# Performance work log

Measured on AMD Instinct MI355X. Metric: run time of the kernel, lower is better.

## Reference

```python
import jax, jax.numpy as jnp
import numpy as np

HID = 10  # hidden_dim


def conv1x1(x, w, b=None):
    # x: [N,C,H,W], w: [O,C] -> [N,O,H,W]
    y = jnp.einsum('oc,nchw->nohw', w, x)
    if b is not None:
        y = y + b[None, :, None, None]
    return y


def gconv1x1(x, w, b=None):
    # grouped 1x1 conv. x: [N,G*ipg,H,W], w: [G,opg,ipg]
    N, C, H, W = x.shape
    G, opg, ipg = w.shape
    xg = x.reshape(N, G, ipg, H, W)
    y = jnp.einsum('goi,ngihw->ngohw', w, xg).reshape(N, G * opg, H, W)
    if b is not None:
        y = y + b[None, :, None, None]
    return y


def _decomp(h_fea, xf, xh, att_w, att_b, w):
    # Decomposition: spatial attention from (fea, xf, xh), gate xf, project.
    att = jax.nn.sigmoid(conv1x1(jnp.concatenate([h_fea, xf, xh], axis=1), att_w, att_b))
    xfh = jax.nn.relu(conv1x1(xf * att, w))
    return xfh, att


def _comp(parts, xh, att_w, att_b, w):
    # Composition: parts [P,N,HID,H,W]; grouped per-part attention then fuse with xh.
    ca = jax.nn.sigmoid(jnp.einsum('pc,pnchw->pnhw', att_w[:, 0], parts) + att_b[:, None, None, None])
    msg = (parts * ca[:, :, None]).sum(0)  # [N,HID,H,W]
    return jax.nn.relu(conv1x1(jnp.concatenate([xh, msg], axis=1), w))


def _update(xh, m0, m1, m2, gate_w, gate_b, cand_w):
    # conv_Update: gated residual update from summed messages.
    cat = jnp.concatenate([xh, m0 + m1 + m2], axis=1)
    g = jax.nn.sigmoid(conv1x1(cat, gate_w, gate_b))
    cand = jax.nn.relu(conv1x1(cat, cand_w))
    return xh * (1.0 - g) + cand * g


def half_graph(h_fea, xh_u, xh_l, xf, xp, pdp_w1, pdp_w2, att_w, att_b,
               compU_att_w, compU_att_b, compU_w,
               compL_att_w, compL_att_b, compL_w,
               decU_att_w, decU_att_b, decU_w,
               decL_att_w, decL_att_b, decL_w,
               updU_gate_w, updU_gate_b, updU_cand_w,
               updL_gate_w, updL_gate_b, updL_cand_w):
    # Part_Dependency: shared trunk then grouped conv -> (dp_u, dp_l)
    t = jax.nn.relu(conv1x1(jnp.concatenate([h_fea, xh_u, xh_l], axis=1), pdp_w1))
    dp = jax.nn.relu(gconv1x1(t, pdp_w2))
    dp_u, dp_l = dp[:, :HID], dp[:, HID:]
    # grouped sigmoid attention over the two half nodes
    a = jax.nn.sigmoid(gconv1x1(jnp.concatenate([xh_u, xh_l], axis=1), att_w, att_b))
    ag_u, ag_l = a[:, 0:1], a[:, 1:2]
    # upper half node
    xphu = _comp(xp[0:4], xh_u, compU_att_w, compU_att_b, compU_w)
    xlh = dp_l * ag_l + xh_u * ag_u  # Pair_Part_Dependency (lower -> upper)
    xfhu, att_u = _decomp(h_fea, xf, xh_u, decU_att_w, decU_att_b, decU_w)
    xh_u_new = _update(xh_u, xphu, xlh, xfhu, updU_gate_w, updU_gate_b, updU_cand_w)
    # lower half node
    xphl = _comp(xp[4:6], xh_l, compL_att_w, compL_att_b, compL_w)
    xuh = dp_u * ag_u + xh_l * ag_l  # Pair_Part_Dependency (upper -> lower)
    xfhl, att_l = _decomp(h_fea, xf, xh_l, decL_att_w, decL_att_b, decL_w)
    xh_l_new = _update(xh_l, xphl, xuh, xfhl, updL_gate_w, updL_gate_b, updL_cand_w)
    return xh_u_new, xh_l_new, att_u, att_l


def setup_inputs() -> dict:
    key = jax.random.key(0)
    N, C, H, W = 8, 256, 128, 128
    ks = jax.random.split(key, 32)
    s = 0.05
    inp = {
        'h_fea': jax.random.normal(ks[0], (N, C, H, W), jnp.float32),
        'xh_u': jax.random.normal(ks[1], (N, HID, H, W), jnp.float32),
        'xh_l': jax.random.normal(ks[2], (N, HID, H, W), jnp.float32),
        'xf': jax.random.normal(ks[3], (N, HID, H, W), jnp.float32),
        'xp': jax.random.normal(ks[4], (6, N, HID, H, W), jnp.float32),
        'pdp_w1': jax.random.normal(ks[5], (2 * HID, C + 2 * HID), jnp.float32) * s,
        'pdp_w2': jax.random.normal(ks[6], (2, HID, HID), jnp.float32) * s,
        'att_w': jax.random.normal(ks[7], (2, 1, HID), jnp.float32) * s,
        'att_b': jnp.zeros((2,), jnp.float32),
        'compU_att_w': jax.random.normal(ks[8], (4, 1, HID), jnp.float32) * s,
        'compU_att_b': jnp.zeros((4,), jnp.float32),
        'compU_w': jax.random.normal(ks[9], (HID, 2 * HID), jnp.float32) * s,
        'compL_att_w': jax.random.normal(ks[10], (2, 1, HID), jnp.float32) * s,
        'compL_att_b': jnp.zeros((2,), jnp.float32),
        'compL_w': jax.random.normal(ks[11], (HID, 2 * HID), jnp.float32) * s,
        'decU_att_w': jax.random.normal(ks[12], (1, C + 2 * HID), jnp.float32) * s,
        'decU_att_b': jnp.zeros((1,), jnp.float32),
        'decU_w': jax.random.normal(ks[13], (HID, HID), jnp.float32) * s,
        'decL_att_w': jax.random.normal(ks[14], (1, C + 2 * HID), jnp.float32) * s,
        'decL_att_b': jnp.zeros((1,), jnp.float32),
        'decL_w': jax.random.normal(ks[15], (HID, HID), jnp.float32) * s,
        'updU_gate_w': jax.random.normal(ks[16], (HID, 2 * HID), jnp.float32) * s,
        'updU_gate_b': jnp.zeros((HID,), jnp.float32),
        'updU_cand_w': jax.random.normal(ks[17], (HID, 2 * HID), jnp.float32) * s,
        'updL_gate_w': jax.random.normal(ks[18], (HID, 2 * HID), jnp.float32) * s,
        'updL_gate_b': jnp.zeros((HID,), jnp.float32),
        'updL_cand_w': jax.random.normal(ks[19], (HID, 2 * HID), jnp.float32) * s,
    }
    return inp


def reference(h_fea, xh_u, xh_l, xf, xp, pdp_w1, pdp_w2, att_w, att_b,
              compU_att_w, compU_att_b, compU_w,
              compL_att_w, compL_att_b, compL_w,
              decU_att_w, decU_att_b, decU_w,
              decL_att_w, decL_att_b, decL_w,
              updU_gate_w, updU_gate_b, updU_cand_w,
              updL_gate_w, updL_gate_b, updL_cand_w):
    return half_graph(h_fea, xh_u, xh_l, xf, xp, pdp_w1, pdp_w2, att_w, att_b,
                      compU_att_w, compU_att_b, compU_w,
                      compL_att_w, compL_att_b, compL_w,
                      decU_att_w, decU_att_b, decU_w,
                      decL_att_w, decL_att_b, decL_w,
                      updU_gate_w, updU_gate_b, updU_cand_w,
                      updL_gate_w, updL_gate_b, updL_cand_w)
```

## Files before the change

### kernel.cpp

```cpp
#include <hip/hip_runtime.h>
#include <stdint.h>

typedef unsigned short u16;
typedef unsigned int   u32;

#define HW   16384
#define NPIX 131072

__device__ __forceinline__ float sigm(float x) { return 1.f / (1.f + __expf(-x)); }

__device__ __forceinline__ float rdlane(float v, int lane) {
    return __int_as_float(__builtin_amdgcn_readlane(__float_as_int(v), lane));
}

__global__ __launch_bounds__(256, 2) void half_graph_fused(
    const float* __restrict__ hf,  const float* __restrict__ xhu, const float* __restrict__ xhl,
    const float* __restrict__ xfg, const float* __restrict__ xpg,
    const float* __restrict__ pdp_w1, const float* __restrict__ pdp_w2,
    const float* __restrict__ att_w,  const float* __restrict__ att_b,
    const float* __restrict__ cU_aw, const float* __restrict__ cU_ab, const float* __restrict__ cU_w,
    const float* __restrict__ cL_aw, const float* __restrict__ cL_ab, const float* __restrict__ cL_w,
    const float* __restrict__ dU_aw, const float* __restrict__ dU_ab, const float* __restrict__ dU_w,
    const float* __restrict__ dL_aw, const float* __restrict__ dL_ab, const float* __restrict__ dL_w,
    const float* __restrict__ uU_gw, const float* __restrict__ uU_gb, const float* __restrict__ uU_cw,
    const float* __restrict__ uL_gw, const float* __restrict__ uL_gb, const float* __restrict__ uL_cw,
    float* __restrict__ out)
{
    const int p  = blockIdx.x * blockDim.x + threadIdx.x;
    const int n  = p >> 14;
    const int hw = p & 16383;
    const int ln = threadIdx.x & 63;

    float xu[10], xl[10], xv[10];
    {
        const float* a = xhu + (size_t)n * 10 * HW + hw;
        const float* b = xhl + (size_t)n * 10 * HW + hw;
        const float* c = xfg + (size_t)n * 10 * HW + hw;
        #pragma unroll
        for (int i = 0; i < 10; ++i) xu[i] = a[i * HW];
        #pragma unroll
        for (int i = 0; i < 10; ++i) xl[i] = b[i * HW];
        #pragma unroll
        for (int i = 0; i < 10; ++i) xv[i] = c[i * HW];
    }

    const float* hfp = hf + (size_t)n * 256 * HW + hw;

    float acc[22];
    #pragma unroll
    for (int o = 0; o < 22; ++o) acc[o] = 0.f;

    float wA[22], wB[22];
    auto prefetch = [&](float (&w)[22], int c0) {
        #pragma unroll
        for (int o = 0; o < 20; ++o) w[o] = pdp_w1[o * 276 + c0 + ln];
        w[20] = dU_aw[c0 + ln];
        w[21] = dL_aw[c0 + ln];
    };
    auto compute = [&](const float (&w)[22], int c0) {
        const float* xp0 = hfp + (size_t)c0 * HW;
        #pragma unroll 8
        for (int cc = 0; cc < 64; ++cc) {
            float x = xp0[cc * HW];
            #pragma unroll
            for (int o = 0; o < 22; ++o)
                acc[o] = fmaf(rdlane(w[o], cc), x, acc[o]);
        }
    };

    prefetch(wA, 0);
    prefetch(wB, 64);
    compute(wA, 0);
    prefetch(wA, 128);
    compute(wB, 64);
    prefetch(wB, 192);
    compute(wA, 128);
    compute(wB, 192);

    const float dU = acc[20], dL = acc[21];

    float t[20];
    #pragma unroll
    for (int o = 0; o < 20; ++o) {
        float s = acc[o];
        #pragma unroll
        for (int i = 0; i < 10; ++i) s = fmaf(pdp_w1[o * 276 + 256 + i], xu[i], s);
        #pragma unroll
        for (int i = 0; i < 10; ++i) s = fmaf(pdp_w1[o * 276 + 266 + i], xl[i], s);
        t[o] = fmaxf(s, 0.f);
    }
    float dpv[20];
    #pragma unroll
    for (int g = 0; g < 2; ++g) {
        #pragma unroll
        for (int o = 0; o < 10; ++o) {
            float s = 0.f;
            #pragma unroll
            for (int i = 0; i < 10; ++i)
                s = fmaf(pdp_w2[(g * 10 + o) * 10 + i], t[g * 10 + i], s);
            dpv[g * 10 + o] = fmaxf(s, 0.f);
        }
    }

    float au_s = att_b[0], al_s = att_b[1];
    #pragma unroll
    for (int i = 0; i < 10; ++i) {
        au_s = fmaf(att_w[i], xu[i], au_s);
        al_s = fmaf(att_w[10 + i], xl[i], al_s);
    }
    const float au = sigm(au_s), al = sigm(al_s);

    float su = dU + dU_ab[0];
    float sl = dL + dL_ab[0];
    #pragma unroll
    for (int i = 0; i < 10; ++i) { su = fmaf(dU_aw[256 + i], xv[i], su); sl = fmaf(dL_aw[256 + i], xv[i], sl); }
    #pragma unroll
    for (int i = 0; i < 10; ++i) { su = fmaf(dU_aw[266 + i], xu[i], su); sl = fmaf(dL_aw[266 + i], xl[i], sl); }
    const float attU = sigm(su), attL = sigm(sl);

    float xfhu[10], xfhl[10];
    #pragma unroll
    for (int o = 0; o < 10; ++o) {
        float a = 0.f, b = 0.f;
        #pragma unroll
        for (int i = 0; i < 10; ++i) {
            a = fmaf(dU_w[o * 10 + i], xv[i], a);
            b = fmaf(dL_w[o * 10 + i], xv[i], b);
        }
        xfhu[o] = fmaxf(attU * a, 0.f);
        xfhl[o] = fmaxf(attL * b, 0.f);
    }

    float msgU[10];
    #pragma unroll
    for (int i = 0; i < 10; ++i) msgU[i] = 0.f;
    #pragma unroll
    for (int pp = 0; pp < 4; ++pp) {
        const float* xq = xpg + (size_t)(pp * 8 + n) * 10 * HW + hw;
        float v[10];
        #pragma unroll
        for (int i = 0; i < 10; ++i) v[i] = xq[i * HW];
        float s = cU_ab[pp];
        #pragma unroll
        for (int i = 0; i < 10; ++i) s = fmaf(cU_aw[pp * 10 + i], v[i], s);
        float ca = sigm(s);
        #pragma unroll
        for (int i = 0; i < 10; ++i) msgU[i] = fmaf(ca, v[i], msgU[i]);
    }
    float xphu[10];
    #pragma unroll
    for (int o = 0; o < 10; ++o) {
        float s = 0.f;
        #pragma unroll
        for (int i = 0; i < 10; ++i) s = fmaf(cU_w[o * 20 + i], xu[i], s);
        #pragma unroll
        for (int i = 0; i < 10; ++i) s = fmaf(cU_w[o * 20 + 10 + i], msgU[i], s);
        xphu[o] = fmaxf(s, 0.f);
    }

    float msgL[10];
    #pragma unroll
    for (int i = 0; i < 10; ++i) msgL[i] = 0.f;
    #pragma unroll
    for (int pp = 4; pp < 6; ++pp) {
        const float* xq = xpg + (size_t)(pp * 8 + n) * 10 * HW + hw;
        float v[10];
        #pragma unroll
        for (int i = 0; i < 10; ++i) v[i] = xq[i * HW];
        float s = cL_ab[pp - 4];
        #pragma unroll
        for (int i = 0; i < 10; ++i) s = fmaf(cL_aw[(pp - 4) * 10 + i], v[i], s);
        float ca = sigm(s);
        #pragma unroll
        for (int i = 0; i < 10; ++i) msgL[i] = fmaf(ca, v[i], msgL[i]);
    }
    float xphl[10];
    #pragma unroll
    for (int o = 0; o < 10; ++o) {
        float s = 0.f;
        #pragma unroll
        for (int i = 0; i < 10; ++i) s = fmaf(cL_w[o * 20 + i], xl[i], s);
        #pragma unroll
        for (int i = 0; i < 10; ++i) s = fmaf(cL_w[o * 20 + 10 + i], msgL[i], s);
        xphl[o] = fmaxf(s, 0.f);
    }

    float outU[10], outL[10];
    {
        float m[10];
        #pragma unroll
        for (int i = 0; i < 10; ++i)
            m[i] = xphu[i] + (dpv[10 + i] * al + xu[i] * au) + xfhu[i];
        #pragma unroll
        for (int o = 0; o < 10; ++o) {
            float gs = uU_gb[o], cs = 0.f;
            #pragma unroll
            for (int i = 0; i < 10; ++i) {
                gs = fmaf(uU_gw[o * 20 + i], xu[i], gs);
                cs = fmaf(uU_cw[o * 20 + i], xu[i], cs);
            }
            #pragma unroll
            for (int i = 0; i < 10; ++i) {
                gs = fmaf(uU_gw[o * 20 + 10 + i], m[i], gs);
                cs = fmaf(uU_cw[o * 20 + 10 + i], m[i], cs);
            }
            float g = sigm(gs), cd = fmaxf(cs, 0.f);
            outU[o] = xu[o] * (1.f - g) + cd * g;
        }
    }
    {
        float m[10];
        #pragma unroll
        for (int i = 0; i < 10; ++i)
            m[i] = xphl[i] + (dpv[i] * au + xl[i] * al) + xfhl[i];
        #pragma unroll
        for (int o = 0; o < 10; ++o) {
            float gs = uL_gb[o], cs = 0.f;
            #pragma unroll
            for (int i = 0; i < 10; ++i) {
                gs = fmaf(uL_gw[o * 20 + i], xl[i], gs);
                cs = fmaf(uL_cw[o * 20 + i], xl[i], cs);
            }
            #pragma unroll
            for (int i = 0; i < 10; ++i) {
                gs = fmaf(uL_gw[o * 20 + 10 + i], m[i], gs);
                cs = fmaf(uL_cw[o * 20 + 10 + i], m[i], cs);
            }
            float g = sigm(gs), cd = fmaxf(cs, 0.f);
            outL[o] = xl[o] * (1.f - g) + cd * g;
        }
    }

    {
        int baseU = n * 10 * HW + hw;
        #pragma unroll
        for (int c = 0; c < 10; ++c) out[baseU + c * HW] = outU[c];
        int baseL = 1310720 + baseU;
        #pragma unroll
        for (int c = 0; c < 10; ++c) out[baseL + c * HW] = outL[c];
        out[2621440 + n * HW + hw] = attU;
        out[2752512 + n * HW + hw] = attL;
    }
}

extern "C" void kernel_launch(void* const* d_in, const int* in_sizes, int n_in,
                              void* d_out, int out_size, void* d_ws, size_t ws_size,
                              hipStream_t stream) {
    (void)in_sizes; (void)n_in; (void)out_size; (void)d_ws; (void)ws_size;
    const float* hf   = (const float*)d_in[0];
    const float* xhu  = (const float*)d_in[1];
    const float* xhl  = (const float*)d_in[2];
    const float* xfg  = (const float*)d_in[3];
    const float* xpg  = (const float*)d_in[4];
    const float* w1   = (const float*)d_in[5];
    const float* w2   = (const float*)d_in[6];
    const float* aw   = (const float*)d_in[7];
    const float* ab   = (const float*)d_in[8];
    const float* cUaw = (const float*)d_in[9];
    const float* cUab = (const float*)d_in[10];
    const float* cUw  = (const float*)d_in[11];
    const float* cLaw = (const float*)d_in[12];
    const float* cLab = (const float*)d_in[13];
    const float* cLw  = (const float*)d_in[14];
    const float* dUaw = (const float*)d_in[15];
    const float* dUab = (const float*)d_in[16];
    const float* dUw  = (const float*)d_in[17];
    const float* dLaw = (const float*)d_in[18];
    const float* dLab = (const float*)d_in[19];
    const float* dLw  = (const float*)d_in[20];
    const float* uUgw = (const float*)d_in[21];
    const float* uUgb = (const float*)d_in[22];
    const float* uUcw = (const float*)d_in[23];
    const float* uLgw = (const float*)d_in[24];
    const float* uLgb = (const float*)d_in[25];
    const float* uLcw = (const float*)d_in[26];

    dim3 grid(NPIX / 256), block(256);
    hipLaunchKernelGGL(half_graph_fused, grid, block, 0, stream,
        hf, xhu, xhl, xfg, xpg, w1, w2, aw, ab,
        cUaw, cUab, cUw, cLaw, cLab, cLw,
        dUaw, dUab, dUw, dLaw, dLab, dLw,
        uUgw, uUgb, uUcw, uLgw, uLgb, uLcw,
        (float*)d_out);
}
```

Before: 298.4 us.

## Use split-fp16 MFMA for 256-channel trunk and split upper/lower work across threads

The 256-channel 1x1 conv over h_fea (22 outputs) moves from scalar FMAs with readlane broadcasts onto 32x32x16 fp16 MFMA. Weights are pre-packed into hi/lo fp16 pairs by a small prep kernel, and activations are split on the fly, using three MFMAs per step to approximate fp32 accuracy. Results pass through shared memory to the epilogue, where each pixel's upper and lower branches are handled by two different threads, halving per-thread register pressure and allowing more waves per SIMD. Costs include an extra kernel launch, workspace use, a block barrier, and error from the split-fp16 approximation.

Result: faster. 278.3 us (-6.7%).

```diff
diff --git a/kernel.cpp b/kernel.cpp
--- a/kernel.cpp
+++ b/kernel.cpp
@@ -1,19 +1,35 @@
 #include <hip/hip_runtime.h>
 #include <stdint.h>
 
+typedef unsigned int   u32;
 typedef unsigned short u16;
-typedef unsigned int   u32;
-
-#define HW   16384
-#define NPIX 131072
+
+#define HW 16384
+
+typedef __attribute__((ext_vector_type(8)))  _Float16 half8;
+typedef __attribute__((ext_vector_type(16))) float    f32x16;
 
 __device__ __forceinline__ float sigm(float x) { return 1.f / (1.f + __expf(-x)); }
 
-__device__ __forceinline__ float rdlane(float v, int lane) {
-    return __int_as_float(__builtin_amdgcn_readlane(__float_as_int(v), lane));
+
+__global__ __launch_bounds__(256) void prep_apack(
+    const float* __restrict__ pdp_w1, const float* __restrict__ dU_aw,
+    const float* __restrict__ dL_aw, _Float16* __restrict__ apack)
+{
+    int idx = blockIdx.x * 256 + threadIdx.x;
+    int s = idx >> 9, rem = idx & 511, l = rem >> 3, j = rem & 7;
+    int o = l & 31, kh = l >> 5;
+    int k = s * 16 + kh * 8 + j;
+    float wv = 0.f;
+    if (o < 20)       wv = pdp_w1[o * 276 + k];
+    else if (o == 20) wv = dU_aw[k];
+    else if (o == 21) wv = dL_aw[k];
+    _Float16 h = (_Float16)wv;
+    apack[idx]        = h;
+    apack[8192 + idx] = (_Float16)(wv - (float)h);
 }
 
-__global__ __launch_bounds__(256, 2) void half_graph_fused(
+__global__ __launch_bounds__(256, 4) void half_graph_fused(
     const float* __restrict__ hf,  const float* __restrict__ xhu, const float* __restrict__ xhl,
     const float* __restrict__ xfg, const float* __restrict__ xpg,
     const float* __restrict__ pdp_w1, const float* __restrict__ pdp_w2,
@@ -24,173 +40,133 @@
     const float* __restrict__ dL_aw, const float* __restrict__ dL_ab, const float* __restrict__ dL_w,
     const float* __restrict__ uU_gw, const float* __restrict__ uU_gb, const float* __restrict__ uU_cw,
     const float* __restrict__ uL_gw, const float* __restrict__ uL_gb, const float* __restrict__ uL_cw,
+    const _Float16* __restrict__ apack,
     float* __restrict__ out)
 {
-    const int p  = blockIdx.x * blockDim.x + threadIdx.x;
-    const int n  = p >> 14;
-    const int hw = p & 16383;
-    const int ln = threadIdx.x & 63;
-
+    const int tid    = threadIdx.x;
+    const int pxbase = blockIdx.x * 128;
+    const int n      = pxbase >> 14;
+    const int hwbase = pxbase & 16383;
+
+    __shared__ float sacc[22][128];
+
+    {
+        const int l   = tid & 63;
+        const int w   = tid >> 6;
+        const int col = l & 31;
+        const int kh  = l >> 5;
+        const float* bp = hf + ((size_t)n * 256 + kh * 8) * HW + (hwbase + w * 32 + col);
+        const half8* ah  = (const half8*)apack;
+        const half8* al8 = ah + 1024;
+        f32x16 acc = {};
+        #pragma unroll 2
+        for (int s = 0; s < 16; ++s) {
+            half8 A_h = ah[s * 64 + l];
+            half8 A_l = al8[s * 64 + l];
+            float x[8];
+            #pragma unroll
+            for (int j = 0; j < 8; ++j) x[j] = bp[(size_t)(s * 16 + j) * HW];
+            half8 B_h, B_l;
+            #pragma unroll
+            for (int j = 0; j < 8; ++j) {
+                _Float16 h = (_Float16)x[j];
+                B_h[j] = h;
+                B_l[j] = (_Float16)(x[j] - (float)h);
+            }
+            acc = __builtin_amdgcn_mfma_f32_32x32x16_f16(A_h, B_h, acc, 0, 0, 0);
+            acc = __builtin_amdgcn_mfma_f32_32x32x16_f16(A_h, B_l, acc, 0, 0, 0);
+            acc = __builtin_amdgcn_mfma_f32_32x32x16_f16(A_l, B_h, acc, 0, 0, 0);
+        }
+        const int ccol = w * 32 + col;
+        #pragma unroll
+        for (int reg = 0; reg < 12; ++reg) {
+            const int r = (reg & 3) + 8 * (reg >> 2) + 4 * kh;
+            if (r < 22) sacc[r][ccol] = acc[reg];
+        }
+    }
+
+    const int q    = tid & 127;
+    const int role = tid >> 7;
+    const int hw   = hwbase + q;
+    const int vb   = n * 10 * HW + hw;
     float xu[10], xl[10], xv[10];
-    {
-        const float* a = xhu + (size_t)n * 10 * HW + hw;
-        const float* b = xhl + (size_t)n * 10 * HW + hw;
-        const float* c = xfg + (size_t)n * 10 * HW + hw;
-        #pragma unroll
-        for (int i = 0; i < 10; ++i) xu[i] = a[i * HW];
-        #pragma unroll
-        for (int i = 0; i < 10; ++i) xl[i] = b[i * HW];
-        #pragma unroll
-        for (int i = 0; i < 10; ++i) xv[i] = c[i * HW];
-    }
-
-    const float* hfp = hf + (size_t)n * 256 * HW + hw;
-
-    float acc[22];
     #pragma unroll
-    for (int o = 0; o < 22; ++o) acc[o] = 0.f;
-
-    float wA[22], wB[22];
-    auto prefetch = [&](float (&w)[22], int c0) {
-        #pragma unroll
-        for (int o = 0; o < 20; ++o) w[o] = pdp_w1[o * 276 + c0 + ln];
-        w[20] = dU_aw[c0 + ln];
-        w[21] = dL_aw[c0 + ln];
-    };
-    auto compute = [&](const float (&w)[22], int c0) {
-        const float* xp0 = hfp + (size_t)c0 * HW;
-        #pragma unroll 8
-        for (int cc = 0; cc < 64; ++cc) {
-            float x = xp0[cc * HW];
-            #pragma unroll
-            for (int o = 0; o < 22; ++o)
-                acc[o] = fmaf(rdlane(w[o], cc), x, acc[o]);
-        }
-    };
-
-    prefetch(wA, 0);
-    prefetch(wB, 64);
-    compute(wA, 0);
-    prefetch(wA, 128);
-    compute(wB, 64);
-    prefetch(wB, 192);
-    compute(wA, 128);
-    compute(wB, 192);
-
-    const float dU = acc[20], dL = acc[21];
-
-    float t[20];
+    for (int i = 0; i < 10; ++i) xu[i] = xhu[vb + i * HW];
     #pragma unroll
-    for (int o = 0; o < 20; ++o) {
-        float s = acc[o];
-        #pragma unroll
-        for (int i = 0; i < 10; ++i) s = fmaf(pdp_w1[o * 276 + 256 + i], xu[i], s);
-        #pragma unroll
-        for (int i = 0; i < 10; ++i) s = fmaf(pdp_w1[o * 276 + 266 + i], xl[i], s);
-        t[o] = fmaxf(s, 0.f);
-    }
-    float dpv[20];
+    for (int i = 0; i < 10; ++i) xl[i] = xhl[vb + i * HW];
     #pragma unroll
-    for (int g = 0; g < 2; ++g) {
-        #pragma unroll
-        for (int o = 0; o < 10; ++o) {
-            float s = 0.f;
-            #pragma unroll
-            for (int i = 0; i < 10; ++i)
-                s = fmaf(pdp_w2[(g * 10 + o) * 10 + i], t[g * 10 + i], s);
-            dpv[g * 10 + o] = fmaxf(s, 0.f);
-        }
-    }
+    for (int i = 0; i < 10; ++i) xv[i] = xfg[vb + i * HW];
+
+    __syncthreads();
 
     float au_s = att_b[0], al_s = att_b[1];
     #pragma unroll
     for (int i = 0; i < 10; ++i) {
-        au_s = fmaf(att_w[i], xu[i], au_s);
+        au_s = fmaf(att_w[i],      xu[i], au_s);
         al_s = fmaf(att_w[10 + i], xl[i], al_s);
     }
     const float au = sigm(au_s), al = sigm(al_s);
 
-    float su = dU + dU_ab[0];
-    float sl = dL + dL_ab[0];
-    #pragma unroll
-    for (int i = 0; i < 10; ++i) { su = fmaf(dU_aw[256 + i], xv[i], su); sl = fmaf(dL_aw[256 + i], xv[i], sl); }
-    #pragma unroll
-    for (int i = 0; i < 10; ++i) { su = fmaf(dU_aw[266 + i], xu[i], su); sl = fmaf(dL_aw[266 + i], xl[i], sl); }
-    const float attU = sigm(su), attL = sigm(sl);
-
-    float xfhu[10], xfhl[10];
-    #pragma unroll
-    for (int o = 0; o < 10; ++o) {
-        float a = 0.f, b = 0.f;
-        #pragma unroll
-        for (int i = 0; i < 10; ++i) {
-            a = fmaf(dU_w[o * 10 + i], xv[i], a);
-            b = fmaf(dL_w[o * 10 + i], xv[i], b);
-        }
-        xfhu[o] = fmaxf(attU * a, 0.f);
-        xfhl[o] = fmaxf(attL * b, 0.f);
-    }
-
-    float msgU[10];
-    #pragma unroll
-    for (int i = 0; i < 10; ++i) msgU[i] = 0.f;
-    #pragma unroll
-    for (int pp = 0; pp < 4; ++pp) {
-        const float* xq = xpg + (size_t)(pp * 8 + n) * 10 * HW + hw;
-        float v[10];
-        #pragma unroll
-        for (int i = 0; i < 10; ++i) v[i] = xq[i * HW];
-        float s = cU_ab[pp];
-        #pragma unroll
-        for (int i = 0; i < 10; ++i) s = fmaf(cU_aw[pp * 10 + i], v[i], s);
-        float ca = sigm(s);
-        #pragma unroll
-        for (int i = 0; i < 10; ++i) msgU[i] = fmaf(ca, v[i], msgU[i]);
-    }
-    float xphu[10];
-    #pragma unroll
-    for (int o = 0; o < 10; ++o) {
-        float s = 0.f;
-        #pragma unroll
-        for (int i = 0; i < 10; ++i) s = fmaf(cU_w[o * 20 + i], xu[i], s);
-        #pragma unroll
-        for (int i = 0; i < 10; ++i) s = fmaf(cU_w[o * 20 + 10 + i], msgU[i], s);
-        xphu[o] = fmaxf(s, 0.f);
-    }
-
-    float msgL[10];
-    #pragma unroll
-    for (int i = 0; i < 10; ++i) msgL[i] = 0.f;
-    #pragma unroll
-    for (int pp = 4; pp < 6; ++pp) {
-        const float* xq = xpg + (size_t)(pp * 8 + n) * 10 * HW + hw;
-        float v[10];
-        #pragma unroll
-        for (int i = 0; i < 10; ++i) v[i] = xq[i * HW];
-        float s = cL_ab[pp - 4];
-        #pragma unroll
-        for (int i = 0; i < 10; ++i) s = fmaf(cL_aw[(pp - 4) * 10 + i], v[i], s);
-        float ca = sigm(s);
-        #pragma unroll
-        for (int i = 0; i < 10; ++i) msgL[i] = fmaf(ca, v[i], msgL[i]);
-    }
-    float xphl[10];
-    #pragma unroll
-    for (int o = 0; o < 10; ++o) {
-        float s = 0.f;
-        #pragma unroll
-        for (int i = 0; i < 10; ++i) s = fmaf(cL_w[o * 20 + i], xl[i], s);
-        #pragma unroll
-        for (int i = 0; i < 10; ++i) s = fmaf(cL_w[o * 20 + 10 + i], msgL[i], s);
-        xphl[o] = fmaxf(s, 0.f);
-    }
-
-    float outU[10], outL[10];
-    {
+    if (role == 0) {
+        float tt[10];
+        #pragma unroll
+        for (int o = 0; o < 10; ++o) {
+            const float* wr = pdp_w1 + (10 + o) * 276;
+            float s = sacc[10 + o][q];
+            #pragma unroll
+            for (int i = 0; i < 10; ++i) s = fmaf(wr[256 + i], xu[i], s);
+            #pragma unroll
+            for (int i = 0; i < 10; ++i) s = fmaf(wr[266 + i], xl[i], s);
+            tt[o] = fmaxf(s, 0.f);
+        }
+        float dpl[10];
+        #pragma unroll
+        for (int o = 0; o < 10; ++o) {
+            float s = 0.f;
+            #pragma unroll
+            for (int i = 0; i < 10; ++i) s = fmaf(pdp_w2[(10 + o) * 10 + i], tt[i], s);
+            dpl[o] = fmaxf(s, 0.f);
+        }
+        float su = sacc[20][q] + dU_ab[0];
+        #pragma unroll
+        for (int i = 0; i < 10; ++i) su = fmaf(dU_aw[256 + i], xv[i], su);
+        #pragma unroll
+        for (int i = 0; i < 10; ++i) su = fmaf(dU_aw[266 + i], xu[i], su);
+        const float attU = sigm(su);
+        float xfh[10];
+        #pragma unroll
+        for (int o = 0; o < 10; ++o) {
+            float a = 0.f;
+            #pragma unroll
+            for (int i = 0; i < 10; ++i) a = fmaf(dU_w[o * 10 + i], xv[i], a);
+            xfh[o] = fmaxf(attU * a, 0.f);
+        }
+        float msg[10];
+        #pragma unroll
+        for (int i = 0; i < 10; ++i) msg[i] = 0.f;
+        #pragma unroll
+        for (int pp = 0; pp < 4; ++pp) {
+            const float* xq = xpg + (size_t)(pp * 8 + n) * 10 * HW + hw;
+            float v[10];
+            #pragma unroll
+            for (int i = 0; i < 10; ++i) v[i] = xq[i * HW];
+            float s = cU_ab[pp];
+            #pragma unroll
+            for (int i = 0; i < 10; ++i) s = fmaf(cU_aw[pp * 10 + i], v[i], s);
+            float ca = sigm(s);
+            #pragma unroll
+            for (int i = 0; i < 10; ++i) msg[i] = fmaf(ca, v[i], msg[i]);
+        }
         float m[10];
         #pragma unroll
-        for (int i = 0; i < 10; ++i)
-            m[i] = xphu[i] + (dpv[10 + i] * al + xu[i] * au) + xfhu[i];
+        for (int o = 0; o < 10; ++o) {
+            float s = 0.f;
+            #pragma unroll
+            for (int i = 0; i < 10; ++i) s = fmaf(cU_w[o * 20 + i],      xu[i],  s);
+            #pragma unroll
+            for (int i = 0; i < 10; ++i) s = fmaf(cU_w[o * 20 + 10 + i], msg[i], s);
+            m[o] = fmaxf(s, 0.f) + fmaf(dpl[o], al, xu[o] * au) + xfh[o];
+        }
         #pragma unroll
         for (int o = 0; o < 10; ++o) {
             float gs = uU_gb[o], cs = 0.f;
@@ -205,14 +181,69 @@
                 cs = fmaf(uU_cw[o * 20 + 10 + i], m[i], cs);
             }
             float g = sigm(gs), cd = fmaxf(cs, 0.f);
-            outU[o] = xu[o] * (1.f - g) + cd * g;
-        }
-    }
-    {
+            out[vb + o * HW] = xu[o] * (1.f - g) + cd * g;
+        }
+        out[2621440 + n * HW + hw] = attU;
+    } else {
+        float tt[10];
+        #pragma unroll
+        for (int o = 0; o < 10; ++o) {
+            const float* wr = pdp_w1 + o * 276;
+            float s = sacc[o][q];
+            #pragma unroll
+            for (int i = 0; i < 10; ++i) s = fmaf(wr[256 + i], xu[i], s);
+            #pragma unroll
+            for (int i = 0; i < 10; ++i) s = fmaf(wr[266 + i], xl[i], s);
+            tt[o] = fmaxf(s, 0.f);
+        }
+        float dpu[10];
+        #pragma unroll
+        for (int o = 0; o < 10; ++o) {
+            float s = 0.f;
+            #pragma unroll
+            for (int i = 0; i < 10; ++i) s = fmaf(pdp_w2[o * 10 + i], tt[i], s);
+            dpu[o] = fmaxf(s, 0.f);
+        }
+        float sl = sacc[21][q] + dL_ab[0];
+        #pragma unroll
+        for (int i = 0; i < 10; ++i) sl = fmaf(dL_aw[256 + i], xv[i], sl);
+        #pragma unroll
+        for (int i = 0; i < 10; ++i) sl = fmaf(dL_aw[266 + i], xl[i], sl);
+        const float attL = sigm(sl);
+        float xfh[10];
+        #pragma unroll
+        for (int o = 0; o < 10; ++o) {
+            float a = 0.f;
+            #pragma unroll
+            for (int i = 0; i < 10; ++i) a = fmaf(dL_w[o * 10 + i], xv[i], a);
+            xfh[o] = fmaxf(attL * a, 0.f);
+        }
+        float msg[10];
+        #pragma unroll
+        for (int i = 0; i < 10; ++i) msg[i] = 0.f;
+        #pragma unroll
+        for (int pp = 0; pp < 2; ++pp) {
+            const float* xq = xpg + (size_t)((pp + 4) * 8 + n) * 10 * HW + hw;
+            float v[10];
+            #pragma unroll
+            for (int i = 0; i < 10; ++i) v[i] = xq[i * HW];
+            float s = cL_ab[pp];
+            #pragma unroll
+            for (int i = 0; i < 10; ++i) s = fmaf(cL_aw[pp * 10 + i], v[i], s);
+            float ca = sigm(s);
+            #pragma unroll
+            for (int i = 0; i < 10; ++i) msg[i] = fmaf(ca, v[i], msg[i]);
+        }
         float m[10];
         #pragma unroll
-        for (int i = 0; i < 10; ++i)
-            m[i] = xphl[i] + (dpv[i] * au + xl[i] * al) + xfhl[i];
+        for (int o = 0; o < 10; ++o) {
+            float s = 0.f;
+            #pragma unroll
+            for (int i = 0; i < 10; ++i) s = fmaf(cL_w[o * 20 + i],      xl[i],  s);
+            #pragma unroll
+            for (int i = 0; i < 10; ++i) s = fmaf(cL_w[o * 20 + 10 + i], msg[i], s);
+            m[o] = fmaxf(s, 0.f) + fmaf(dpu[o], au, xl[o] * al) + xfh[o];
+        }
         #pragma unroll
         for (int o = 0; o < 10; ++o) {
             float gs = uL_gb[o], cs = 0.f;
@@ -227,18 +258,8 @@
                 cs = fmaf(uL_cw[o * 20 + 10 + i], m[i], cs);
             }
             float g = sigm(gs), cd = fmaxf(cs, 0.f);
-            outL[o] = xl[o] * (1.f - g) + cd * g;
-        }
-    }
-
-    {
-        int baseU = n * 10 * HW + hw;
-        #pragma unroll
-        for (int c = 0; c < 10; ++c) out[baseU + c * HW] = outU[c];
-        int baseL = 1310720 + baseU;
-        #pragma unroll
-        for (int c = 0; c < 10; ++c) out[baseL + c * HW] = outL[c];
-        out[2621440 + n * HW + hw] = attU;
+            out[1310720 + vb + o * HW] = xl[o] * (1.f - g) + cd * g;
+        }
         out[2752512 + n * HW + hw] = attL;
     }
 }
@@ -246,7 +267,7 @@
 extern "C" void kernel_launch(void* const* d_in, const int* in_sizes, int n_in,
                               void* d_out, int out_size, void* d_ws, size_t ws_size,
                               hipStream_t stream) {
-    (void)in_sizes; (void)n_in; (void)out_size; (void)d_ws; (void)ws_size;
+    (void)in_sizes; (void)n_in; (void)out_size; (void)ws_size;
     const float* hf   = (const float*)d_in[0];
     const float* xhu  = (const float*)d_in[1];
     const float* xhl  = (const float*)d_in[2];
@@ -275,11 +296,15 @@
     const float* uLgb = (const float*)d_in[25];
     const float* uLcw = (const float*)d_in[26];
 
-    dim3 grid(NPIX / 256), block(256);
-    hipLaunchKernelGGL(half_graph_fused, grid, block, 0, stream,
+    _Float16* apack = (_Float16*)d_ws;
+
+    hipLaunchKernelGGL(prep_apack, dim3(32), dim3(256), 0, stream,
+                       w1, dUaw, dLaw, apack);
+    hipLaunchKernelGGL(half_graph_fused, dim3(1024), dim3(256), 0, stream,
         hf, xhu, xhl, xfg, xpg, w1, w2, aw, ab,
         cUaw, cUab, cUw, cLaw, cLab, cLw,
         dUaw, dUab, dUw, dLaw, dLab, dLw,
         uUgw, uUgb, uUcw, uLgw, uLgb, uLcw,
+        (const _Float16*)apack,
         (float*)d_out);
 }
```
